# Kernel optimization log

Hardware: AMD Instinct MI355X
Metric: run time of the kernel (lower is better)

The kernel has to match this reference:

```python
import jax, jax.numpy as jnp
import numpy as np

SEQ_LEN = 64  # config.SEQ_LEN
T, B, N, D = 256, 128, 4, 2
H_HIS, H_INT = 32, 8


def _uniform(key, shape, k):
    return jax.random.uniform(key, shape, jnp.float32, -k, k)


def setup_inputs() -> dict:
    key = jax.random.key(0)
    ks = jax.random.split(key, 12)
    kh = 1.0 / np.sqrt(H_HIS)
    ki = 1.0 / np.sqrt(H_INT)
    ko = 1.0 / np.sqrt(40)
    return {
        "inputs": jax.random.normal(ks[0], (T, B, N, D), jnp.float32),
        # history LSTM (input 2 -> hidden 32), gate order i,f,g,o like torch
        "Wih_his": _uniform(ks[1], (4 * H_HIS, D), kh),
        "Whh_his": _uniform(ks[2], (4 * H_HIS, H_HIS), kh),
        "bih_his": _uniform(ks[3], (4 * H_HIS,), kh),
        "bhh_his": _uniform(ks[4], (4 * H_HIS,), kh),
        # interaction LSTM (input 2 -> hidden 8)
        "Wih_int": _uniform(ks[5], (4 * H_INT, D), ki),
        "Whh_int": _uniform(ks[6], (4 * H_INT, H_INT), ki),
        "bih_int": _uniform(ks[7], (4 * H_INT,), ki),
        "bhh_int": _uniform(ks[8], (4 * H_INT,), ki),
        # output Linear(40 -> 2)
        "W_out": _uniform(ks[9], (2, H_HIS + H_INT), ko),
        "b_out": _uniform(ks[10], (2,), ko),
    }


def _lstm_windows(x_w, valid, Wih, Whh, bih, bhh):
    """Run an LSTM over L steps for T independent windows at once.
    x_w: [L, Tw, B, d]  inputs per step (leading padding for short windows)
    valid: [L, Tw] bool; while False the state is held at zero, which is
    exactly equivalent to starting the window fresh at its first valid step.
    Returns final hidden state h: [Tw, B, H].
    """
    H = Whh.shape[1]
    Tw, Bb = x_w.shape[1], x_w.shape[2]
    b = bih + bhh

    def step(carry, xs):
        h, c = carry
        x, v = xs
        g = x @ Wih.T + h @ Whh.T + b            # [Tw, B, 4H]
        i, f, gg, o = jnp.split(g, 4, axis=-1)
        c_new = jax.nn.sigmoid(f) * c + jax.nn.sigmoid(i) * jnp.tanh(gg)
        h_new = jax.nn.sigmoid(o) * jnp.tanh(c_new)
        m = v[:, None, None]
        return (jnp.where(m, h_new, 0.0), jnp.where(m, c_new, 0.0)), None

    init = (jnp.zeros((Tw, Bb, H), x_w.dtype), jnp.zeros((Tw, Bb, H), x_w.dtype))
    (h, _), _ = jax.lax.scan(step, init, (x_w, valid))
    return h


def reference(inputs, Wih_his, Whh_his, bih_his, bhh_his,
              Wih_int, Whh_int, bih_int, bhh_int, W_out, b_out):
    Tt, Bb, Nn, Dd = inputs.shape
    L = SEQ_LEN
    # window index for output frame t: frames t-L+1 .. t (clipped; invalid masked)
    t = jnp.arange(Tt)[:, None]
    s = jnp.arange(L)[None, :]
    idx = t - (L - 1) + s                      # [T, L]
    valid = (idx >= 0)
    idx_c = jnp.clip(idx, 0, Tt - 1)
    x_his = inputs[:, :, -1, :][idx_c]         # [T, L, B, d] (ego / last node)
    x_int = inputs[:, :, 0, :][idx_c]          # [T, L, B, d] (interaction node)
    x_his = jnp.transpose(x_his, (1, 0, 2, 3))  # [L, T, B, d]
    x_int = jnp.transpose(x_int, (1, 0, 2, 3))
    v = jnp.transpose(valid)                   # [L, T]

    h_his = _lstm_windows(x_his, v, Wih_his, Whh_his, bih_his, bhh_his)  # [T,B,32]
    h_int = _lstm_windows(x_int, v, Wih_int, Whh_int, bih_int, bhh_int)  # [T,B,8]
    emb = jnp.concatenate([h_his, h_int], axis=-1)                       # [T,B,40]
    return emb @ W_out.T + b_out                                         # [T,B,2]
```

## Files before the change

kernel.cpp:

```cpp
#include <hip/hip_runtime.h>


typedef float v2f __attribute__((ext_vector_type(2)));
typedef float v4f __attribute__((ext_vector_type(4)));
typedef _Float16 h8v __attribute__((ext_vector_type(8)));

static __device__ __forceinline__ float fexp2(float x) {
    return __builtin_amdgcn_exp2f(x);
}
static __device__ __forceinline__ float frcp(float x) {
    return __builtin_amdgcn_rcpf(x);
}
static __device__ __forceinline__ unsigned short f2h(float f) {
    _Float16 h = (_Float16)f;
    unsigned short u;
    __builtin_memcpy(&u, &h, 2);
    return u;
}
static __device__ __forceinline__ float h2f(unsigned short u) {
    _Float16 h;
    __builtin_memcpy(&h, &u, 2);
    return (float)h;
}

#define LOG2E    1.442695041f
#define TWOLOG2E 2.885390082f

__global__ __launch_bounds__(256) void prep_kernel(
    const float* __restrict__ Wih_his, const float* __restrict__ Whh_his,
    const float* __restrict__ bih_his, const float* __restrict__ bhh_his,
    const float* __restrict__ Wih_int, const float* __restrict__ Whh_int,
    const float* __restrict__ bih_int, const float* __restrict__ bhh_int,
    float* __restrict__ ws)
{
    const int i = blockIdx.x * 256 + threadIdx.x;
    if (i < 4832) {
    } else if (i < 4960) {
        const int p = i - 4832;
        const int T = p >> 4, n = p & 15;
        const int gi = T >> 1, u = 2 * n + (T & 1);
        const int r = gi * 32 + u;
        const float s = (gi == 2) ? -TWOLOG2E : -LOG2E;
        ws[5120 + p] = (bih_his[r] + bhh_his[r]) * s;
    } else if (i < 5216) {
        const int e = i - 4960;
        const int p = e >> 1, comp = e & 1;
        const int T = p >> 4, n = p & 15;
        const int gi = T >> 1, u = 2 * n + (T & 1);
        const int r = gi * 32 + u;
        const float s = (gi == 2) ? -TWOLOG2E : -LOG2E;
        ws[5376 + e] = Wih_his[r * 2 + comp] * s;
    } else if (i < 9312) {
        const int e = i - 5216;
        const int p = e >> 5, k = e & 31;
        const int T = p >> 4, n = p & 15;
        const int gi = T >> 1, u = 2 * n + (T & 1);
        const int r = gi * 32 + u;
        const float s = (gi == 2) ? -TWOLOG2E : -LOG2E;
        reinterpret_cast<unsigned short*>(ws)[11776 + e] =
            f2h(Whh_his[r * 32 + k] * s);
    } else if (i < 9344) {
        const int s = i - 9312;
        const int T = s >> 4, m = s & 15, r = m & 3;
        const int gate = (4 * T + r) >> 1, unit = 2 * (m >> 2) + (r & 1);
        const int orig = gate * 8 + unit;
        const float sc = (gate == 2) ? -TWOLOG2E : -LOG2E;
        ws[7936 + s] = (bih_int[orig] + bhh_int[orig]) * sc;
    } else if (i < 9408) {
        const int e = i - 9344;
        const int s = e >> 1, comp = e & 1;
        const int T = s >> 4, m = s & 15, r = m & 3;
        const int gate = (4 * T + r) >> 1, unit = 2 * (m >> 2) + (r & 1);
        const int orig = gate * 8 + unit;
        const float sc = (gate == 2) ? -TWOLOG2E : -LOG2E;
        ws[7968 + e] = Wih_int[orig * 2 + comp] * sc;
    } else if (i < 9664) {
        const int e = i - 9408;
        const int s = e >> 3, k = e & 7;
        const int T = s >> 4, m = s & 15, r = m & 3;
        const int gate = (4 * T + r) >> 1, unit = 2 * (m >> 2) + (r & 1);
        const int orig = gate * 8 + unit;
        const float sc = (gate == 2) ? -TWOLOG2E : -LOG2E;
        const float w = Whh_int[orig * 8 + k] * sc;
        const unsigned short hi = f2h(w);
        const unsigned short lo = f2h(w - h2f(hi));
        reinterpret_cast<unsigned short*>(ws)[16128 + e] = hi;
        reinterpret_cast<unsigned short*>(ws)[8704 + e]  = lo;
    }
}

__global__ __launch_bounds__(64) void intm_kernel(
    const float* __restrict__ inp, const float* __restrict__ ws,
    const float* __restrict__ W_out, float* __restrict__ eInt)
{
    const int lane = threadIdx.x;
    const int n    = lane & 15;
    const int q    = lane >> 4;
    const int Wd   = blockIdx.x;
    const int t    = Wd >> 3;
    const int bg   = Wd & 7;
    const int nsteps = (t >= 63) ? 64 : (t + 1);
    const int tau0   = (t >= 63) ? (t - 63) : 0;

    h8v Ai[2];
    {
        const h8v* wah = reinterpret_cast<const h8v*>(
            reinterpret_cast<const unsigned short*>(ws) + 16128);
        const h8v* wal = reinterpret_cast<const h8v*>(
            reinterpret_cast<const unsigned short*>(ws) + 8704);
#pragma unroll
        for (int T = 0; T < 2; ++T) {
            const h8v vh = wah[T * 16 + n];
            const h8v vl = wal[T * 16 + n];
            Ai[T] = (q < 2) ? vh : vl;
        }
    }

    float cb[2][4], cw0v[2][4], cw1v[2][4];
#pragma unroll
    for (int T = 0; T < 2; ++T)
#pragma unroll
        for (int r = 0; r < 4; ++r) {
            const int s = T * 16 + q * 4 + r;
            cb[T][r]   = ws[7936 + s];
            cw0v[T][r] = ws[7968 + 2 * s];
            cw1v[T][r] = ws[7968 + 2 * s + 1];
        }

    const int chain = bg * 16 + n;
    const float* xp = inp + tau0 * 1024 + chain * 8;
    float2 xv = *reinterpret_cast<const float2*>(xp);
    float2 x1 = make_float2(0.f, 0.f);
    if (nsteps > 1) x1 = *reinterpret_cast<const float2*>(xp + 1024);
    xp += 2048;

    union BU { unsigned u[4]; h8v h; } bf;
    bf.u[0] = bf.u[1] = bf.u[2] = bf.u[3] = 0;

    float cI0 = 0.f, cI1 = 0.f, h0 = 0.f, h1 = 0.f;

#pragma unroll 1
    for (int s = 0; s < nsteps; ++s) {
        float2 x2 = make_float2(0.f, 0.f);
        if (s + 2 < nsteps)
            x2 = *reinterpret_cast<const float2*>(xp);
        xp += 1024;

        v4f C0, C1;
#pragma unroll
        for (int r = 0; r < 4; ++r) {
            C0[r] = fmaf(cw1v[0][r], xv.y, fmaf(cw0v[0][r], xv.x, cb[0][r]));
            C1[r] = fmaf(cw1v[1][r], xv.y, fmaf(cw0v[1][r], xv.x, cb[1][r]));
        }
        const v4f D0 = __builtin_amdgcn_mfma_f32_16x16x32_f16(Ai[0], bf.h, C0, 0, 0, 0);
        const v4f D1 = __builtin_amdgcn_mfma_f32_16x16x32_f16(Ai[1], bf.h, C1, 0, 0, 0);

        {
            const float si = frcp(1.f + fexp2(D0[0]));
            const float sf = frcp(1.f + fexp2(D0[2]));
            const float tg = fmaf(2.f, frcp(1.f + fexp2(D1[0])), -1.f);
            const float so = frcp(1.f + fexp2(D1[2]));
            const float cn = fmaf(sf, cI0, si * tg);
            cI0 = cn;
            h0 = so * fmaf(-2.f, frcp(1.f + fexp2(TWOLOG2E * cn)), 1.f);
        }
        {
            const float si = frcp(1.f + fexp2(D0[1]));
            const float sf = frcp(1.f + fexp2(D0[3]));
            const float tg = fmaf(2.f, frcp(1.f + fexp2(D1[1])), -1.f);
            const float so = frcp(1.f + fexp2(D1[3]));
            const float cn = fmaf(sf, cI1, si * tg);
            cI1 = cn;
            h1 = so * fmaf(-2.f, frcp(1.f + fexp2(TWOLOG2E * cn)), 1.f);
        }

        if (s + 1 < nsteps) {
            const unsigned short h0h = f2h(h0), h1h = f2h(h1);
            const float h0l = h0 - h2f(h0h);
            const float h1l = h1 - h2f(h1h);
            const unsigned pkh = ((unsigned)h1h << 16) | h0h;
            const unsigned pkl = ((unsigned)f2h(h1l) << 16) | f2h(h0l);
#pragma unroll
            for (int d = 0; d < 4; ++d) {
                const unsigned uh = (unsigned)__shfl((int)pkh, d * 16 + n);
                const unsigned ul = (unsigned)__shfl((int)pkl, d * 16 + n);
                bf.u[d] = (q & 1) ? ul : uh;
            }
        }

        xv = x1;
        x1 = x2;
    }

    const float wo0a = W_out[32 + 2 * q], wo0b = W_out[33 + 2 * q];
    const float wo1a = W_out[72 + 2 * q], wo1b = W_out[73 + 2 * q];
    float e0 = fmaf(wo0b, h1, wo0a * h0);
    float e1 = fmaf(wo1b, h1, wo1a * h0);
    e0 += __shfl_xor(e0, 16); e1 += __shfl_xor(e1, 16);
    e0 += __shfl_xor(e0, 32); e1 += __shfl_xor(e1, 32);
    if (lane < 16) {
        float2 o; o.x = e0; o.y = e1;
        reinterpret_cast<float2*>(eInt)[t * 128 + chain] = o;
    }
}

__global__ __launch_bounds__(64) void his_kernel(
    const float* __restrict__ inp, const float* __restrict__ ws,
    const float* __restrict__ W_out, const float* __restrict__ b_out,
    const float* __restrict__ eInt, float* __restrict__ out)
{
    __shared__ __align__(16) unsigned short hm[2][16][40];

    const int lane = threadIdx.x;
    const int n    = lane & 15;
    const int quad = lane >> 4;
    const int Wd   = blockIdx.x;
    const int t    = Wd >> 3;
    const int bg   = Wd & 7;
    const int nsteps = (t >= 63) ? 64 : (t + 1);
    const int tau0   = (t >= 63) ? (t - 63) : 0;

    h8v Bf[8];
    {
        const h8v* wb = reinterpret_cast<const h8v*>(
            reinterpret_cast<const unsigned short*>(ws) + 11776);
#pragma unroll
        for (int T = 0; T < 8; ++T) Bf[T] = wb[(T * 16 + n) * 4 + quad];
    }
    float cb[8], cw0[8], cw1[8];
#pragma unroll
    for (int T = 0; T < 8; ++T) {
        const int p = T * 16 + n;
        cb[T]  = ws[5120 + p];
        cw0[T] = ws[5376 + 2 * p];
        cw1[T] = ws[5376 + 2 * p + 1];
    }

    const int bbase = bg * 16 + quad * 4;
    const float* xp = inp + tau0 * 1024 + bbase * 8 + 6;
    float2 xc[4];
#pragma unroll
    for (int r = 0; r < 4; ++r)
        xc[r] = *reinterpret_cast<const float2*>(xp + r * 8);
    xp += 1024;

    h8v Af = {};
    float cs[4][2] = {};
    float h0[4] = {}, h1[4] = {};

#pragma unroll 1
    for (int s = 0; s < nsteps; ++s) {
        float2 xn[4];
        if (s + 1 < nsteps) {
#pragma unroll
            for (int r = 0; r < 4; ++r)
                xn[r] = *reinterpret_cast<const float2*>(xp + r * 8);
        } else {
#pragma unroll
            for (int r = 0; r < 4; ++r) xn[r] = make_float2(0.f, 0.f);
        }
        xp += 1024;

        v4f D[8];
#pragma unroll
        for (int T = 0; T < 8; ++T) {
            v4f C;
#pragma unroll
            for (int r = 0; r < 4; ++r)
                C[r] = fmaf(cw1[T], xc[r].y, fmaf(cw0[T], xc[r].x, cb[T]));
            D[T] = __builtin_amdgcn_mfma_f32_16x16x32_f16(Af, Bf[T], C, 0, 0, 0);
        }

#pragma unroll
        for (int r = 0; r < 4; ++r) {
            {
                const float si = frcp(1.f + fexp2(D[0][r]));
                const float sf = frcp(1.f + fexp2(D[2][r]));
                const float tg = fmaf(2.f, frcp(1.f + fexp2(D[4][r])), -1.f);
                const float so = frcp(1.f + fexp2(D[6][r]));
                const float cn = fmaf(sf, cs[r][0], si * tg);
                cs[r][0] = cn;
                h0[r] = so * fmaf(-2.f, frcp(1.f + fexp2(TWOLOG2E * cn)), 1.f);
            }
            {
                const float si = frcp(1.f + fexp2(D[1][r]));
                const float sf = frcp(1.f + fexp2(D[3][r]));
                const float tg = fmaf(2.f, frcp(1.f + fexp2(D[5][r])), -1.f);
                const float so = frcp(1.f + fexp2(D[7][r]));
                const float cn = fmaf(sf, cs[r][1], si * tg);
                cs[r][1] = cn;
                h1[r] = so * fmaf(-2.f, frcp(1.f + fexp2(TWOLOG2E * cn)), 1.f);
            }
        }

        if (s + 1 < nsteps) {
            const int bf = s & 1;
#pragma unroll
            for (int r = 0; r < 4; ++r) {
                const unsigned pk =
                    ((unsigned)f2h(h1[r]) << 16) | f2h(h0[r]);
                *reinterpret_cast<unsigned*>(&hm[bf][quad * 4 + r][2 * n]) = pk;
            }
            __builtin_amdgcn_wave_barrier();
            asm volatile("s_waitcnt lgkmcnt(0)" ::: "memory");
            __builtin_amdgcn_wave_barrier();
            Af = *reinterpret_cast<const h8v*>(&hm[bf][n][quad * 8]);
        }

#pragma unroll
        for (int r = 0; r < 4; ++r) xc[r] = xn[r];
    }

    const float wo0a = W_out[2 * n],      wo0b = W_out[2 * n + 1];
    const float wo1a = W_out[40 + 2 * n], wo1b = W_out[40 + 2 * n + 1];
    float e0[4], e1[4];
#pragma unroll
    for (int r = 0; r < 4; ++r) {
        e0[r] = fmaf(wo0b, h1[r], wo0a * h0[r]);
        e1[r] = fmaf(wo1b, h1[r], wo1a * h0[r]);
#pragma unroll
        for (int m = 1; m <= 8; m <<= 1) {
            e0[r] += __shfl_xor(e0[r], m);
            e1[r] += __shfl_xor(e1[r], m);
        }
    }
    if (n == 0) {
        const float bo0 = b_out[0], bo1 = b_out[1];
#pragma unroll
        for (int r = 0; r < 4; ++r) {
            const int chain = t * 128 + bbase + r;
            const float2 ei = reinterpret_cast<const float2*>(eInt)[chain];
            float2 o;
            o.x = e0[r] + ei.x + bo0;
            o.y = e1[r] + ei.y + bo1;
            reinterpret_cast<float2*>(out)[chain] = o;
        }
    }
}

extern "C" void kernel_launch(void* const* d_in, const int* in_sizes, int n_in,
                              void* d_out, int out_size, void* d_ws, size_t ws_size,
                              hipStream_t stream) {
    const float* inp     = (const float*)d_in[0];
    const float* Wih_his = (const float*)d_in[1];
    const float* Whh_his = (const float*)d_in[2];
    const float* bih_his = (const float*)d_in[3];
    const float* bhh_his = (const float*)d_in[4];
    const float* Wih_int = (const float*)d_in[5];
    const float* Whh_int = (const float*)d_in[6];
    const float* bih_int = (const float*)d_in[7];
    const float* bhh_int = (const float*)d_in[8];
    const float* W_out   = (const float*)d_in[9];
    const float* b_out   = (const float*)d_in[10];
    float* out  = (float*)d_out;
    float* ws   = (float*)d_ws;
    float* eInt = ws + 8192;

    prep_kernel<<<dim3(38), dim3(256), 0, stream>>>(
        Wih_his, Whh_his, bih_his, bhh_his,
        Wih_int, Whh_int, bih_int, bhh_int, ws);

    intm_kernel<<<dim3(2048), dim3(64), 0, stream>>>(inp, ws, W_out, eInt);

    his_kernel<<<dim3(2048), dim3(64), 0, stream>>>(
        inp, ws, W_out, b_out, eInt, out);
}
```

Baseline: 197.9 us.

## Fuse interaction LSTM into history LSTM kernel to share launch and overlap chains

Merges the separate interaction-LSTM kernel into the history-LSTM kernel so each wave runs both recurrences in the same step loop. The interaction embedding is combined through lane shuffles instead of a global scratch round trip. This removes one kernel launch and lets the independent interaction MFMA/transcendental chain fill latency gaps in the history chain. It raises register pressure per wave, which may reduce occupancy or lengthen each step.

```diff
diff --git a/kernel.cpp b/kernel.cpp
--- a/kernel.cpp
+++ b/kernel.cpp
@@ -89,125 +89,10 @@
     }
 }
 
-__global__ __launch_bounds__(64) void intm_kernel(
-    const float* __restrict__ inp, const float* __restrict__ ws,
-    const float* __restrict__ W_out, float* __restrict__ eInt)
-{
-    const int lane = threadIdx.x;
-    const int n    = lane & 15;
-    const int q    = lane >> 4;
-    const int Wd   = blockIdx.x;
-    const int t    = Wd >> 3;
-    const int bg   = Wd & 7;
-    const int nsteps = (t >= 63) ? 64 : (t + 1);
-    const int tau0   = (t >= 63) ? (t - 63) : 0;
-
-    h8v Ai[2];
-    {
-        const h8v* wah = reinterpret_cast<const h8v*>(
-            reinterpret_cast<const unsigned short*>(ws) + 16128);
-        const h8v* wal = reinterpret_cast<const h8v*>(
-            reinterpret_cast<const unsigned short*>(ws) + 8704);
-#pragma unroll
-        for (int T = 0; T < 2; ++T) {
-            const h8v vh = wah[T * 16 + n];
-            const h8v vl = wal[T * 16 + n];
-            Ai[T] = (q < 2) ? vh : vl;
-        }
-    }
-
-    float cb[2][4], cw0v[2][4], cw1v[2][4];
-#pragma unroll
-    for (int T = 0; T < 2; ++T)
-#pragma unroll
-        for (int r = 0; r < 4; ++r) {
-            const int s = T * 16 + q * 4 + r;
-            cb[T][r]   = ws[7936 + s];
-            cw0v[T][r] = ws[7968 + 2 * s];
-            cw1v[T][r] = ws[7968 + 2 * s + 1];
-        }
-
-    const int chain = bg * 16 + n;
-    const float* xp = inp + tau0 * 1024 + chain * 8;
-    float2 xv = *reinterpret_cast<const float2*>(xp);
-    float2 x1 = make_float2(0.f, 0.f);
-    if (nsteps > 1) x1 = *reinterpret_cast<const float2*>(xp + 1024);
-    xp += 2048;
-
-    union BU { unsigned u[4]; h8v h; } bf;
-    bf.u[0] = bf.u[1] = bf.u[2] = bf.u[3] = 0;
-
-    float cI0 = 0.f, cI1 = 0.f, h0 = 0.f, h1 = 0.f;
-
-#pragma unroll 1
-    for (int s = 0; s < nsteps; ++s) {
-        float2 x2 = make_float2(0.f, 0.f);
-        if (s + 2 < nsteps)
-            x2 = *reinterpret_cast<const float2*>(xp);
-        xp += 1024;
-
-        v4f C0, C1;
-#pragma unroll
-        for (int r = 0; r < 4; ++r) {
-            C0[r] = fmaf(cw1v[0][r], xv.y, fmaf(cw0v[0][r], xv.x, cb[0][r]));
-            C1[r] = fmaf(cw1v[1][r], xv.y, fmaf(cw0v[1][r], xv.x, cb[1][r]));
-        }
-        const v4f D0 = __builtin_amdgcn_mfma_f32_16x16x32_f16(Ai[0], bf.h, C0, 0, 0, 0);
-        const v4f D1 = __builtin_amdgcn_mfma_f32_16x16x32_f16(Ai[1], bf.h, C1, 0, 0, 0);
-
-        {
-            const float si = frcp(1.f + fexp2(D0[0]));
-            const float sf = frcp(1.f + fexp2(D0[2]));
-            const float tg = fmaf(2.f, frcp(1.f + fexp2(D1[0])), -1.f);
-            const float so = frcp(1.f + fexp2(D1[2]));
-            const float cn = fmaf(sf, cI0, si * tg);
-            cI0 = cn;
-            h0 = so * fmaf(-2.f, frcp(1.f + fexp2(TWOLOG2E * cn)), 1.f);
-        }
-        {
-            const float si = frcp(1.f + fexp2(D0[1]));
-            const float sf = frcp(1.f + fexp2(D0[3]));
-            const float tg = fmaf(2.f, frcp(1.f + fexp2(D1[1])), -1.f);
-            const float so = frcp(1.f + fexp2(D1[3]));
-            const float cn = fmaf(sf, cI1, si * tg);
-            cI1 = cn;
-            h1 = so * fmaf(-2.f, frcp(1.f + fexp2(TWOLOG2E * cn)), 1.f);
-        }
-
-        if (s + 1 < nsteps) {
-            const unsigned short h0h = f2h(h0), h1h = f2h(h1);
-            const float h0l = h0 - h2f(h0h);
-            const float h1l = h1 - h2f(h1h);
-            const unsigned pkh = ((unsigned)h1h << 16) | h0h;
-            const unsigned pkl = ((unsigned)f2h(h1l) << 16) | f2h(h0l);
-#pragma unroll
-            for (int d = 0; d < 4; ++d) {
-                const unsigned uh = (unsigned)__shfl((int)pkh, d * 16 + n);
-                const unsigned ul = (unsigned)__shfl((int)pkl, d * 16 + n);
-                bf.u[d] = (q & 1) ? ul : uh;
-            }
-        }
-
-        xv = x1;
-        x1 = x2;
-    }
-
-    const float wo0a = W_out[32 + 2 * q], wo0b = W_out[33 + 2 * q];
-    const float wo1a = W_out[72 + 2 * q], wo1b = W_out[73 + 2 * q];
-    float e0 = fmaf(wo0b, h1, wo0a * h0);
-    float e1 = fmaf(wo1b, h1, wo1a * h0);
-    e0 += __shfl_xor(e0, 16); e1 += __shfl_xor(e1, 16);
-    e0 += __shfl_xor(e0, 32); e1 += __shfl_xor(e1, 32);
-    if (lane < 16) {
-        float2 o; o.x = e0; o.y = e1;
-        reinterpret_cast<float2*>(eInt)[t * 128 + chain] = o;
-    }
-}
-
-__global__ __launch_bounds__(64) void his_kernel(
+__global__ __launch_bounds__(64) void fused_kernel(
     const float* __restrict__ inp, const float* __restrict__ ws,
     const float* __restrict__ W_out, const float* __restrict__ b_out,
-    const float* __restrict__ eInt, float* __restrict__ out)
+    float* __restrict__ out)
 {
     __shared__ __align__(16) unsigned short hm[2][16][40];
 
@@ -236,6 +121,30 @@
         cw1[T] = ws[5376 + 2 * p + 1];
     }
 
+    h8v Ai[2];
+    {
+        const h8v* wah = reinterpret_cast<const h8v*>(
+            reinterpret_cast<const unsigned short*>(ws) + 16128);
+        const h8v* wal = reinterpret_cast<const h8v*>(
+            reinterpret_cast<const unsigned short*>(ws) + 8704);
+#pragma unroll
+        for (int T = 0; T < 2; ++T) {
+            const h8v vh = wah[T * 16 + n];
+            const h8v vl = wal[T * 16 + n];
+            Ai[T] = (quad < 2) ? vh : vl;
+        }
+    }
+    float icb[2][4], icw0[2][4], icw1[2][4];
+#pragma unroll
+    for (int T = 0; T < 2; ++T)
+#pragma unroll
+        for (int r = 0; r < 4; ++r) {
+            const int s = T * 16 + quad * 4 + r;
+            icb[T][r]  = ws[7936 + s];
+            icw0[T][r] = ws[7968 + 2 * s];
+            icw1[T][r] = ws[7968 + 2 * s + 1];
+        }
+
     const int bbase = bg * 16 + quad * 4;
     const float* xp = inp + tau0 * 1024 + bbase * 8 + 6;
     float2 xc[4];
@@ -244,22 +153,33 @@
         xc[r] = *reinterpret_cast<const float2*>(xp + r * 8);
     xp += 1024;
 
+    const int ichain = bg * 16 + n;
+    const float* ixp = inp + tau0 * 1024 + ichain * 8;
+    float2 ixv = *reinterpret_cast<const float2*>(ixp);
+    ixp += 1024;
+
     h8v Af = {};
     float cs[4][2] = {};
     float h0[4] = {}, h1[4] = {};
+    union BU { unsigned u[4]; h8v h; } bfr;
+    bfr.u[0] = bfr.u[1] = bfr.u[2] = bfr.u[3] = 0;
+    float cI0 = 0.f, cI1 = 0.f, ih0 = 0.f, ih1 = 0.f;
 
 #pragma unroll 1
     for (int s = 0; s < nsteps; ++s) {
         float2 xn[4];
+        float2 ixn = make_float2(0.f, 0.f);
         if (s + 1 < nsteps) {
 #pragma unroll
             for (int r = 0; r < 4; ++r)
                 xn[r] = *reinterpret_cast<const float2*>(xp + r * 8);
+            ixn = *reinterpret_cast<const float2*>(ixp);
         } else {
 #pragma unroll
             for (int r = 0; r < 4; ++r) xn[r] = make_float2(0.f, 0.f);
         }
         xp += 1024;
+        ixp += 1024;
 
         v4f D[8];
 #pragma unroll
@@ -269,6 +189,37 @@
             for (int r = 0; r < 4; ++r)
                 C[r] = fmaf(cw1[T], xc[r].y, fmaf(cw0[T], xc[r].x, cb[T]));
             D[T] = __builtin_amdgcn_mfma_f32_16x16x32_f16(Af, Bf[T], C, 0, 0, 0);
+        }
+
+        v4f iD0, iD1;
+        {
+            v4f C0, C1;
+#pragma unroll
+            for (int r = 0; r < 4; ++r) {
+                C0[r] = fmaf(icw1[0][r], ixv.y, fmaf(icw0[0][r], ixv.x, icb[0][r]));
+                C1[r] = fmaf(icw1[1][r], ixv.y, fmaf(icw0[1][r], ixv.x, icb[1][r]));
+            }
+            iD0 = __builtin_amdgcn_mfma_f32_16x16x32_f16(Ai[0], bfr.h, C0, 0, 0, 0);
+            iD1 = __builtin_amdgcn_mfma_f32_16x16x32_f16(Ai[1], bfr.h, C1, 0, 0, 0);
+        }
+
+        {
+            const float si = frcp(1.f + fexp2(iD0[0]));
+            const float sf = frcp(1.f + fexp2(iD0[2]));
+            const float tg = fmaf(2.f, frcp(1.f + fexp2(iD1[0])), -1.f);
+            const float so = frcp(1.f + fexp2(iD1[2]));
+            const float cn = fmaf(sf, cI0, si * tg);
+            cI0 = cn;
+            ih0 = so * fmaf(-2.f, frcp(1.f + fexp2(TWOLOG2E * cn)), 1.f);
+        }
+        {
+            const float si = frcp(1.f + fexp2(iD0[1]));
+            const float sf = frcp(1.f + fexp2(iD0[3]));
+            const float tg = fmaf(2.f, frcp(1.f + fexp2(iD1[1])), -1.f);
+            const float so = frcp(1.f + fexp2(iD1[3]));
+            const float cn = fmaf(sf, cI1, si * tg);
+            cI1 = cn;
+            ih1 = so * fmaf(-2.f, frcp(1.f + fexp2(TWOLOG2E * cn)), 1.f);
         }
 
 #pragma unroll
@@ -294,21 +245,45 @@
         }
 
         if (s + 1 < nsteps) {
-            const int bf = s & 1;
+            {
+                const unsigned short h0h = f2h(ih0), h1h = f2h(ih1);
+                const float h0l = ih0 - h2f(h0h);
+                const float h1l = ih1 - h2f(h1h);
+                const unsigned pkh = ((unsigned)h1h << 16) | h0h;
+                const unsigned pkl = ((unsigned)f2h(h1l) << 16) | f2h(h0l);
+#pragma unroll
+                for (int d = 0; d < 4; ++d) {
+                    const unsigned uh = (unsigned)__shfl((int)pkh, d * 16 + n);
+                    const unsigned ul = (unsigned)__shfl((int)pkl, d * 16 + n);
+                    bfr.u[d] = (quad & 1) ? ul : uh;
+                }
+            }
+            const int bfi = s & 1;
 #pragma unroll
             for (int r = 0; r < 4; ++r) {
                 const unsigned pk =
                     ((unsigned)f2h(h1[r]) << 16) | f2h(h0[r]);
-                *reinterpret_cast<unsigned*>(&hm[bf][quad * 4 + r][2 * n]) = pk;
+                *reinterpret_cast<unsigned*>(&hm[bfi][quad * 4 + r][2 * n]) = pk;
             }
             __builtin_amdgcn_wave_barrier();
             asm volatile("s_waitcnt lgkmcnt(0)" ::: "memory");
             __builtin_amdgcn_wave_barrier();
-            Af = *reinterpret_cast<const h8v*>(&hm[bf][n][quad * 8]);
+            Af = *reinterpret_cast<const h8v*>(&hm[bfi][n][quad * 8]);
         }
 
 #pragma unroll
         for (int r = 0; r < 4; ++r) xc[r] = xn[r];
+        ixv = ixn;
+    }
+
+    float ie0, ie1;
+    {
+        const float wo0a = W_out[32 + 2 * quad], wo0b = W_out[33 + 2 * quad];
+        const float wo1a = W_out[72 + 2 * quad], wo1b = W_out[73 + 2 * quad];
+        ie0 = fmaf(wo0b, ih1, wo0a * ih0);
+        ie1 = fmaf(wo1b, ih1, wo1a * ih0);
+        ie0 += __shfl_xor(ie0, 16); ie1 += __shfl_xor(ie1, 16);
+        ie0 += __shfl_xor(ie0, 32); ie1 += __shfl_xor(ie1, 32);
     }
 
     const float wo0a = W_out[2 * n],      wo0b = W_out[2 * n + 1];
@@ -324,15 +299,22 @@
             e1[r] += __shfl_xor(e1[r], m);
         }
     }
+
+    float g0[4], g1[4];
+#pragma unroll
+    for (int r = 0; r < 4; ++r) {
+        g0[r] = __shfl(ie0, quad * 4 + r);
+        g1[r] = __shfl(ie1, quad * 4 + r);
+    }
+
     if (n == 0) {
         const float bo0 = b_out[0], bo1 = b_out[1];
 #pragma unroll
         for (int r = 0; r < 4; ++r) {
             const int chain = t * 128 + bbase + r;
-            const float2 ei = reinterpret_cast<const float2*>(eInt)[chain];
             float2 o;
-            o.x = e0[r] + ei.x + bo0;
-            o.y = e1[r] + ei.y + bo1;
+            o.x = e0[r] + g0[r] + bo0;
+            o.y = e1[r] + g1[r] + bo1;
             reinterpret_cast<float2*>(out)[chain] = o;
         }
     }
@@ -354,14 +336,11 @@
     const float* b_out   = (const float*)d_in[10];
     float* out  = (float*)d_out;
     float* ws   = (float*)d_ws;
-    float* eInt = ws + 8192;
 
     prep_kernel<<<dim3(38), dim3(256), 0, stream>>>(
         Wih_his, Whh_his, bih_his, bhh_his,
         Wih_int, Whh_int, bih_int, bhh_int, ws);
 
-    intm_kernel<<<dim3(2048), dim3(64), 0, stream>>>(inp, ws, W_out, eInt);
-
-    his_kernel<<<dim3(2048), dim3(64), 0, stream>>>(
-        inp, ws, W_out, b_out, eInt, out);
-}
+    fused_kernel<<<dim3(2048), dim3(64), 0, stream>>>(
+        inp, ws, W_out, b_out, out);
+}
```

Result: slower. 238.3 us (+20.4%).

## Swap MFMA operand roles and fold input/bias projection into MFMAs

Applied to the files above, without the earlier changes.

Both LSTM kernels now put weights in the A operand and the hidden state in the B operand, so each lane keeps its own chain's hidden units in registers. The history kernel no longer needs the LDS round trip and wave barriers between steps, and the interaction kernel no longer needs the per-step lane shuffles. The input and bias terms are also computed by extra MFMAs against hi/lo fp16-split inputs with a constant-one column, replacing the per-step scalar FMAs. The cost is twice as many MFMAs per step in the history kernel and more fp16 splitting work per step, with some precision risk from fp16 hi/lo splitting.

```diff
diff --git a/kernel.cpp b/kernel.cpp
--- a/kernel.cpp
+++ b/kernel.cpp
@@ -1,7 +1,6 @@
 #include <hip/hip_runtime.h>
 
 
-typedef float v2f __attribute__((ext_vector_type(2)));
 typedef float v4f __attribute__((ext_vector_type(4)));
 typedef _Float16 h8v __attribute__((ext_vector_type(8)));
 
@@ -25,6 +24,7 @@
 
 #define LOG2E    1.442695041f
 #define TWOLOG2E 2.885390082f
+#define H16ONE   0x3C00u
 
 __global__ __launch_bounds__(256) void prep_kernel(
     const float* __restrict__ Wih_his, const float* __restrict__ Whh_his,
@@ -34,62 +34,68 @@
     float* __restrict__ ws)
 {
     const int i = blockIdx.x * 256 + threadIdx.x;
-    if (i < 4832) {
-    } else if (i < 4960) {
-        const int p = i - 4832;
-        const int T = p >> 4, n = p & 15;
-        const int gi = T >> 1, u = 2 * n + (T & 1);
-        const int r = gi * 32 + u;
-        const float s = (gi == 2) ? -TWOLOG2E : -LOG2E;
-        ws[5120 + p] = (bih_his[r] + bhh_his[r]) * s;
-    } else if (i < 5216) {
-        const int e = i - 4960;
-        const int p = e >> 1, comp = e & 1;
-        const int T = p >> 4, n = p & 15;
-        const int gi = T >> 1, u = 2 * n + (T & 1);
-        const int r = gi * 32 + u;
-        const float s = (gi == 2) ? -TWOLOG2E : -LOG2E;
-        ws[5376 + e] = Wih_his[r * 2 + comp] * s;
-    } else if (i < 9312) {
-        const int e = i - 5216;
-        const int p = e >> 5, k = e & 31;
-        const int T = p >> 4, n = p & 15;
-        const int gi = T >> 1, u = 2 * n + (T & 1);
-        const int r = gi * 32 + u;
-        const float s = (gi == 2) ? -TWOLOG2E : -LOG2E;
-        reinterpret_cast<unsigned short*>(ws)[11776 + e] =
-            f2h(Whh_his[r * 32 + k] * s);
-    } else if (i < 9344) {
-        const int s = i - 9312;
-        const int T = s >> 4, m = s & 15, r = m & 3;
-        const int gate = (4 * T + r) >> 1, unit = 2 * (m >> 2) + (r & 1);
-        const int orig = gate * 8 + unit;
-        const float sc = (gate == 2) ? -TWOLOG2E : -LOG2E;
-        ws[7936 + s] = (bih_int[orig] + bhh_int[orig]) * sc;
-    } else if (i < 9408) {
-        const int e = i - 9344;
-        const int s = e >> 1, comp = e & 1;
-        const int T = s >> 4, m = s & 15, r = m & 3;
-        const int gate = (4 * T + r) >> 1, unit = 2 * (m >> 2) + (r & 1);
-        const int orig = gate * 8 + unit;
-        const float sc = (gate == 2) ? -TWOLOG2E : -LOG2E;
-        ws[7968 + e] = Wih_int[orig * 2 + comp] * sc;
-    } else if (i < 9664) {
-        const int e = i - 9408;
-        const int s = e >> 3, k = e & 7;
-        const int T = s >> 4, m = s & 15, r = m & 3;
-        const int gate = (4 * T + r) >> 1, unit = 2 * (m >> 2) + (r & 1);
-        const int orig = gate * 8 + unit;
-        const float sc = (gate == 2) ? -TWOLOG2E : -LOG2E;
-        const float w = Whh_int[orig * 8 + k] * sc;
-        const unsigned short hi = f2h(w);
-        const unsigned short lo = f2h(w - h2f(hi));
-        reinterpret_cast<unsigned short*>(ws)[16128 + e] = hi;
-        reinterpret_cast<unsigned short*>(ws)[8704 + e]  = lo;
-    }
-}
-
-__global__ __launch_bounds__(64) void intm_kernel(
+    unsigned short* wsu = reinterpret_cast<unsigned short*>(ws);
+
+    if (i < 4096) {
+        const int T = i >> 9, m = (i >> 5) & 15, k = i & 31;
+        const int g = T >> 1;
+        const int u = ((m >> 2) << 3) + ((T & 1) << 2) + (m & 3);
+        const int orig = g * 32 + u;
+        const float s = (g == 2) ? -TWOLOG2E : -LOG2E;
+        wsu[i] = f2h(Whh_his[orig * 32 + k] * s);
+    } else if (i < 8192) {
+        const int e = i - 4096;
+        const int T = e >> 9, m = (e >> 5) & 15, k = e & 31;
+        const int g = T >> 1;
+        const int u = ((m >> 2) << 3) + ((T & 1) << 2) + (m & 3);
+        const int orig = g * 32 + u;
+        const float s = (g == 2) ? -TWOLOG2E : -LOG2E;
+        const float w0 = Wih_his[orig * 2] * s;
+        const float w1 = Wih_his[orig * 2 + 1] * s;
+        const float b  = (bih_his[orig] + bhh_his[orig]) * s;
+        unsigned short v = 0;
+        switch (k) {
+            case 0: v = f2h(w0); break;
+            case 1: v = f2h(w1); break;
+            case 2: v = f2h(b);  break;
+            case 3: v = f2h(w0 - h2f(f2h(w0))); break;
+            case 4: v = f2h(w1 - h2f(f2h(w1))); break;
+            case 5: v = f2h(b  - h2f(f2h(b)));  break;
+            case 6: v = f2h(w0); break;
+            case 7: v = f2h(w1); break;
+            default: v = 0; break;
+        }
+        wsu[4096 + e] = v;
+    } else if (i < 9216) {
+        const int e = i - 8192;
+        const int T = e >> 9, m = (e >> 5) & 15, k = e & 31;
+        const int q = k >> 3, j = k & 7;
+        const int g = 2 * T + ((m & 3) >> 1);
+        const int u = 2 * (m >> 2) + (m & 1);
+        const int orig = g * 8 + u;
+        const float s = (g == 2) ? -TWOLOG2E : -LOG2E;
+        unsigned short v = 0;
+        if (j < 6) {
+            const int col = 2 * q + (j & 1);
+            const float w = Whh_int[orig * 8 + col] * s;
+            v = (j == 2 || j == 3) ? f2h(w - h2f(f2h(w))) : f2h(w);
+        } else {
+            const int comp = j & 1;
+            if (q <= 1) {
+                v = f2h(Wih_int[orig * 2 + comp] * s);
+            } else if (q == 2) {
+                const float w = Wih_int[orig * 2 + comp] * s;
+                v = f2h(w - h2f(f2h(w)));
+            } else {
+                const float b = (bih_int[orig] + bhh_int[orig]) * s;
+                v = (comp == 0) ? f2h(b) : f2h(b - h2f(f2h(b)));
+            }
+        }
+        wsu[8192 + e] = v;
+    }
+}
+
+__global__ __launch_bounds__(64) void intw_kernel(
     const float* __restrict__ inp, const float* __restrict__ ws,
     const float* __restrict__ W_out, float* __restrict__ eInt)
 {
@@ -102,58 +108,42 @@
     const int nsteps = (t >= 63) ? 64 : (t + 1);
     const int tau0   = (t >= 63) ? (t - 63) : 0;
 
-    h8v Ai[2];
-    {
-        const h8v* wah = reinterpret_cast<const h8v*>(
-            reinterpret_cast<const unsigned short*>(ws) + 16128);
-        const h8v* wal = reinterpret_cast<const h8v*>(
-            reinterpret_cast<const unsigned short*>(ws) + 8704);
-#pragma unroll
-        for (int T = 0; T < 2; ++T) {
-            const h8v vh = wah[T * 16 + n];
-            const h8v vl = wal[T * 16 + n];
-            Ai[T] = (q < 2) ? vh : vl;
-        }
-    }
-
-    float cb[2][4], cw0v[2][4], cw1v[2][4];
-#pragma unroll
-    for (int T = 0; T < 2; ++T)
-#pragma unroll
-        for (int r = 0; r < 4; ++r) {
-            const int s = T * 16 + q * 4 + r;
-            cb[T][r]   = ws[7936 + s];
-            cw0v[T][r] = ws[7968 + 2 * s];
-            cw1v[T][r] = ws[7968 + 2 * s + 1];
-        }
+    const unsigned short* wsu = reinterpret_cast<const unsigned short*>(ws);
+    const h8v* wa = reinterpret_cast<const h8v*>(wsu + 8192);
+    h8v AI[2];
+#pragma unroll
+    for (int T = 0; T < 2; ++T) AI[T] = wa[T * 64 + n * 4 + q];
 
     const int chain = bg * 16 + n;
     const float* xp = inp + tau0 * 1024 + chain * 8;
     float2 xv = *reinterpret_cast<const float2*>(xp);
-    float2 x1 = make_float2(0.f, 0.f);
-    if (nsteps > 1) x1 = *reinterpret_cast<const float2*>(xp + 1024);
-    xp += 2048;
-
-    union BU { unsigned u[4]; h8v h; } bf;
-    bf.u[0] = bf.u[1] = bf.u[2] = bf.u[3] = 0;
-
-    float cI0 = 0.f, cI1 = 0.f, h0 = 0.f, h1 = 0.f;
+    xp += 1024;
+
+    union BU { unsigned u[4]; h8v h; } bh;
+    bh.u[0] = bh.u[1] = bh.u[2] = bh.u[3] = 0;
+
+    float cI0 = 0.f, cI1 = 0.f, ih0 = 0.f, ih1 = 0.f;
 
 #pragma unroll 1
     for (int s = 0; s < nsteps; ++s) {
-        float2 x2 = make_float2(0.f, 0.f);
-        if (s + 2 < nsteps)
-            x2 = *reinterpret_cast<const float2*>(xp);
+        float2 xn = make_float2(0.f, 0.f);
+        if (s + 1 < nsteps)
+            xn = *reinterpret_cast<const float2*>(xp);
         xp += 1024;
 
-        v4f C0, C1;
-#pragma unroll
-        for (int r = 0; r < 4; ++r) {
-            C0[r] = fmaf(cw1v[0][r], xv.y, fmaf(cw0v[0][r], xv.x, cb[0][r]));
-            C1[r] = fmaf(cw1v[1][r], xv.y, fmaf(cw0v[1][r], xv.x, cb[1][r]));
-        }
-        const v4f D0 = __builtin_amdgcn_mfma_f32_16x16x32_f16(Ai[0], bf.h, C0, 0, 0, 0);
-        const v4f D1 = __builtin_amdgcn_mfma_f32_16x16x32_f16(Ai[1], bf.h, C1, 0, 0, 0);
+        {
+            const unsigned short xh = f2h(xv.x), yh = f2h(xv.y);
+            const unsigned short xl = f2h(xv.x - h2f(xh));
+            const unsigned short yl = f2h(xv.y - h2f(yh));
+            const unsigned pkh = ((unsigned)yh << 16) | xh;
+            const unsigned pkl = ((unsigned)yl << 16) | xl;
+            bh.u[3] = (q == 3) ? ((H16ONE << 16) | H16ONE)
+                               : ((q == 1) ? pkl : pkh);
+        }
+
+        const v4f z = {0.f, 0.f, 0.f, 0.f};
+        const v4f D0 = __builtin_amdgcn_mfma_f32_16x16x32_f16(AI[0], bh.h, z, 0, 0, 0);
+        const v4f D1 = __builtin_amdgcn_mfma_f32_16x16x32_f16(AI[1], bh.h, z, 0, 0, 0);
 
         {
             const float si = frcp(1.f + fexp2(D0[0]));
@@ -162,7 +152,7 @@
             const float so = frcp(1.f + fexp2(D1[2]));
             const float cn = fmaf(sf, cI0, si * tg);
             cI0 = cn;
-            h0 = so * fmaf(-2.f, frcp(1.f + fexp2(TWOLOG2E * cn)), 1.f);
+            ih0 = so * fmaf(-2.f, frcp(1.f + fexp2(TWOLOG2E * cn)), 1.f);
         }
         {
             const float si = frcp(1.f + fexp2(D0[1]));
@@ -171,31 +161,25 @@
             const float so = frcp(1.f + fexp2(D1[3]));
             const float cn = fmaf(sf, cI1, si * tg);
             cI1 = cn;
-            h1 = so * fmaf(-2.f, frcp(1.f + fexp2(TWOLOG2E * cn)), 1.f);
-        }
-
-        if (s + 1 < nsteps) {
-            const unsigned short h0h = f2h(h0), h1h = f2h(h1);
-            const float h0l = h0 - h2f(h0h);
-            const float h1l = h1 - h2f(h1h);
-            const unsigned pkh = ((unsigned)h1h << 16) | h0h;
-            const unsigned pkl = ((unsigned)f2h(h1l) << 16) | f2h(h0l);
-#pragma unroll
-            for (int d = 0; d < 4; ++d) {
-                const unsigned uh = (unsigned)__shfl((int)pkh, d * 16 + n);
-                const unsigned ul = (unsigned)__shfl((int)pkl, d * 16 + n);
-                bf.u[d] = (q & 1) ? ul : uh;
-            }
-        }
-
-        xv = x1;
-        x1 = x2;
+            ih1 = so * fmaf(-2.f, frcp(1.f + fexp2(TWOLOG2E * cn)), 1.f);
+        }
+
+        {
+            const unsigned short hh0 = f2h(ih0), hh1 = f2h(ih1);
+            const unsigned short hl0 = f2h(ih0 - h2f(hh0));
+            const unsigned short hl1 = f2h(ih1 - h2f(hh1));
+            bh.u[0] = ((unsigned)hh1 << 16) | hh0;
+            bh.u[1] = bh.u[0];
+            bh.u[2] = ((unsigned)hl1 << 16) | hl0;
+        }
+
+        xv = xn;
     }
 
     const float wo0a = W_out[32 + 2 * q], wo0b = W_out[33 + 2 * q];
     const float wo1a = W_out[72 + 2 * q], wo1b = W_out[73 + 2 * q];
-    float e0 = fmaf(wo0b, h1, wo0a * h0);
-    float e1 = fmaf(wo1b, h1, wo1a * h0);
+    float e0 = fmaf(wo0b, ih1, wo0a * ih0);
+    float e1 = fmaf(wo1b, ih1, wo1a * ih0);
     e0 += __shfl_xor(e0, 16); e1 += __shfl_xor(e1, 16);
     e0 += __shfl_xor(e0, 32); e1 += __shfl_xor(e1, 32);
     if (lane < 16) {
@@ -204,137 +188,108 @@
     }
 }
 
-__global__ __launch_bounds__(64) void his_kernel(
+__global__ __launch_bounds__(64) void hisw_kernel(
     const float* __restrict__ inp, const float* __restrict__ ws,
     const float* __restrict__ W_out, const float* __restrict__ b_out,
     const float* __restrict__ eInt, float* __restrict__ out)
 {
-    __shared__ __align__(16) unsigned short hm[2][16][40];
-
     const int lane = threadIdx.x;
     const int n    = lane & 15;
-    const int quad = lane >> 4;
+    const int q    = lane >> 4;
     const int Wd   = blockIdx.x;
     const int t    = Wd >> 3;
     const int bg   = Wd & 7;
     const int nsteps = (t >= 63) ? 64 : (t + 1);
     const int tau0   = (t >= 63) ? (t - 63) : 0;
 
-    h8v Bf[8];
-    {
-        const h8v* wb = reinterpret_cast<const h8v*>(
-            reinterpret_cast<const unsigned short*>(ws) + 11776);
-#pragma unroll
-        for (int T = 0; T < 8; ++T) Bf[T] = wb[(T * 16 + n) * 4 + quad];
-    }
-    float cb[8], cw0[8], cw1[8];
+    const unsigned short* wsu = reinterpret_cast<const unsigned short*>(ws);
+    const h8v* wa = reinterpret_cast<const h8v*>(wsu);
+    const h8v* wx = reinterpret_cast<const h8v*>(wsu + 4096);
+    h8v AW[8], AX[8];
 #pragma unroll
     for (int T = 0; T < 8; ++T) {
-        const int p = T * 16 + n;
-        cb[T]  = ws[5120 + p];
-        cw0[T] = ws[5376 + 2 * p];
-        cw1[T] = ws[5376 + 2 * p + 1];
-    }
-
-    const int bbase = bg * 16 + quad * 4;
-    const float* xp = inp + tau0 * 1024 + bbase * 8 + 6;
-    float2 xc[4];
-#pragma unroll
-    for (int r = 0; r < 4; ++r)
-        xc[r] = *reinterpret_cast<const float2*>(xp + r * 8);
+        AW[T] = wa[T * 64 + n * 4 + q];
+        AX[T] = wx[T * 64 + n * 4 + q];
+    }
+
+    const int chain = bg * 16 + n;
+    const float* xp = inp + tau0 * 1024 + chain * 8 + 6;
+    float2 xv = *reinterpret_cast<const float2*>(xp);
     xp += 1024;
 
-    h8v Af = {};
-    float cs[4][2] = {};
-    float h0[4] = {}, h1[4] = {};
+    union BU { unsigned u[4]; h8v h; } bh;
+    bh.u[0] = bh.u[1] = bh.u[2] = bh.u[3] = 0;
+    float c[8] = {0.f, 0.f, 0.f, 0.f, 0.f, 0.f, 0.f, 0.f};
+    float h[8] = {0.f, 0.f, 0.f, 0.f, 0.f, 0.f, 0.f, 0.f};
 
 #pragma unroll 1
     for (int s = 0; s < nsteps; ++s) {
-        float2 xn[4];
-        if (s + 1 < nsteps) {
-#pragma unroll
-            for (int r = 0; r < 4; ++r)
-                xn[r] = *reinterpret_cast<const float2*>(xp + r * 8);
-        } else {
-#pragma unroll
-            for (int r = 0; r < 4; ++r) xn[r] = make_float2(0.f, 0.f);
-        }
+        float2 xn = make_float2(0.f, 0.f);
+        if (s + 1 < nsteps)
+            xn = *reinterpret_cast<const float2*>(xp);
         xp += 1024;
 
+        union BU bx;
+        {
+            const unsigned short xh = f2h(xv.x), yh = f2h(xv.y);
+            const unsigned short xl = f2h(xv.x - h2f(xh));
+            const unsigned short yl = f2h(xv.y - h2f(yh));
+            bx.u[0] = ((unsigned)yh << 16) | xh;
+            bx.u[1] = ((unsigned)xh << 16) | H16ONE;
+            bx.u[2] = (H16ONE << 16) | yh;
+            bx.u[3] = ((unsigned)yl << 16) | xl;
+            if (q != 0) { bx.u[0] = 0; bx.u[1] = 0; bx.u[2] = 0; bx.u[3] = 0; }
+        }
+
+        const v4f z = {0.f, 0.f, 0.f, 0.f};
         v4f D[8];
 #pragma unroll
         for (int T = 0; T < 8; ++T) {
-            v4f C;
-#pragma unroll
-            for (int r = 0; r < 4; ++r)
-                C[r] = fmaf(cw1[T], xc[r].y, fmaf(cw0[T], xc[r].x, cb[T]));
-            D[T] = __builtin_amdgcn_mfma_f32_16x16x32_f16(Af, Bf[T], C, 0, 0, 0);
-        }
-
-#pragma unroll
-        for (int r = 0; r < 4; ++r) {
-            {
-                const float si = frcp(1.f + fexp2(D[0][r]));
-                const float sf = frcp(1.f + fexp2(D[2][r]));
-                const float tg = fmaf(2.f, frcp(1.f + fexp2(D[4][r])), -1.f);
-                const float so = frcp(1.f + fexp2(D[6][r]));
-                const float cn = fmaf(sf, cs[r][0], si * tg);
-                cs[r][0] = cn;
-                h0[r] = so * fmaf(-2.f, frcp(1.f + fexp2(TWOLOG2E * cn)), 1.f);
+            const v4f cx = __builtin_amdgcn_mfma_f32_16x16x32_f16(AX[T], bx.h, z, 0, 0, 0);
+            D[T] = __builtin_amdgcn_mfma_f32_16x16x32_f16(AW[T], bh.h, cx, 0, 0, 0);
+        }
+
+#pragma unroll
+        for (int hi = 0; hi < 2; ++hi) {
+#pragma unroll
+            for (int lo = 0; lo < 4; ++lo) {
+                const int ww = hi * 4 + lo;
+                const float si = frcp(1.f + fexp2(D[hi][lo]));
+                const float sf = frcp(1.f + fexp2(D[2 + hi][lo]));
+                const float tg = fmaf(2.f, frcp(1.f + fexp2(D[4 + hi][lo])), -1.f);
+                const float so = frcp(1.f + fexp2(D[6 + hi][lo]));
+                const float cn = fmaf(sf, c[ww], si * tg);
+                c[ww] = cn;
+                h[ww] = so * fmaf(-2.f, frcp(1.f + fexp2(TWOLOG2E * cn)), 1.f);
             }
-            {
-                const float si = frcp(1.f + fexp2(D[1][r]));
-                const float sf = frcp(1.f + fexp2(D[3][r]));
-                const float tg = fmaf(2.f, frcp(1.f + fexp2(D[5][r])), -1.f);
-                const float so = frcp(1.f + fexp2(D[7][r]));
-                const float cn = fmaf(sf, cs[r][1], si * tg);
-                cs[r][1] = cn;
-                h1[r] = so * fmaf(-2.f, frcp(1.f + fexp2(TWOLOG2E * cn)), 1.f);
-            }
-        }
-
-        if (s + 1 < nsteps) {
-            const int bf = s & 1;
-#pragma unroll
-            for (int r = 0; r < 4; ++r) {
-                const unsigned pk =
-                    ((unsigned)f2h(h1[r]) << 16) | f2h(h0[r]);
-                *reinterpret_cast<unsigned*>(&hm[bf][quad * 4 + r][2 * n]) = pk;
-            }
-            __builtin_amdgcn_wave_barrier();
-            asm volatile("s_waitcnt lgkmcnt(0)" ::: "memory");
-            __builtin_amdgcn_wave_barrier();
-            Af = *reinterpret_cast<const h8v*>(&hm[bf][n][quad * 8]);
-        }
-
-#pragma unroll
-        for (int r = 0; r < 4; ++r) xc[r] = xn[r];
-    }
-
-    const float wo0a = W_out[2 * n],      wo0b = W_out[2 * n + 1];
-    const float wo1a = W_out[40 + 2 * n], wo1b = W_out[40 + 2 * n + 1];
-    float e0[4], e1[4];
-#pragma unroll
-    for (int r = 0; r < 4; ++r) {
-        e0[r] = fmaf(wo0b, h1[r], wo0a * h0[r]);
-        e1[r] = fmaf(wo1b, h1[r], wo1a * h0[r]);
-#pragma unroll
-        for (int m = 1; m <= 8; m <<= 1) {
-            e0[r] += __shfl_xor(e0[r], m);
-            e1[r] += __shfl_xor(e1[r], m);
-        }
-    }
-    if (n == 0) {
-        const float bo0 = b_out[0], bo1 = b_out[1];
-#pragma unroll
-        for (int r = 0; r < 4; ++r) {
-            const int chain = t * 128 + bbase + r;
-            const float2 ei = reinterpret_cast<const float2*>(eInt)[chain];
-            float2 o;
-            o.x = e0[r] + ei.x + bo0;
-            o.y = e1[r] + ei.y + bo1;
-            reinterpret_cast<float2*>(out)[chain] = o;
-        }
+        }
+
+#pragma unroll
+        for (int d = 0; d < 4; ++d)
+            bh.u[d] = ((unsigned)f2h(h[2 * d + 1]) << 16) | f2h(h[2 * d]);
+
+        xv = xn;
+    }
+
+    const v4f w0a = *reinterpret_cast<const v4f*>(W_out + q * 8);
+    const v4f w0b = *reinterpret_cast<const v4f*>(W_out + q * 8 + 4);
+    const v4f w1a = *reinterpret_cast<const v4f*>(W_out + 40 + q * 8);
+    const v4f w1b = *reinterpret_cast<const v4f*>(W_out + 40 + q * 8 + 4);
+    float e0 = 0.f, e1 = 0.f;
+#pragma unroll
+    for (int j = 0; j < 4; ++j) {
+        e0 = fmaf(w0a[j], h[j], fmaf(w0b[j], h[4 + j], e0));
+        e1 = fmaf(w1a[j], h[j], fmaf(w1b[j], h[4 + j], e1));
+    }
+    e0 += __shfl_xor(e0, 16); e1 += __shfl_xor(e1, 16);
+    e0 += __shfl_xor(e0, 32); e1 += __shfl_xor(e1, 32);
+
+    if (lane < 16) {
+        const float2 ei = reinterpret_cast<const float2*>(eInt)[t * 128 + chain];
+        float2 o;
+        o.x = e0 + ei.x + b_out[0];
+        o.y = e1 + ei.y + b_out[1];
+        reinterpret_cast<float2*>(out)[t * 128 + chain] = o;
     }
 }
 
@@ -356,12 +311,12 @@
     float* ws   = (float*)d_ws;
     float* eInt = ws + 8192;
 
-    prep_kernel<<<dim3(38), dim3(256), 0, stream>>>(
+    prep_kernel<<<dim3(36), dim3(256), 0, stream>>>(
         Wih_his, Whh_his, bih_his, bhh_his,
         Wih_int, Whh_int, bih_int, bhh_int, ws);
 
-    intm_kernel<<<dim3(2048), dim3(64), 0, stream>>>(inp, ws, W_out, eInt);
-
-    his_kernel<<<dim3(2048), dim3(64), 0, stream>>>(
+    intw_kernel<<<dim3(2048), dim3(64), 0, stream>>>(inp, ws, W_out, eInt);
+
+    hisw_kernel<<<dim3(2048), dim3(64), 0, stream>>>(
         inp, ws, W_out, b_out, eInt, out);
 }
```

New measurement: 185.9 us. 6.1% less time.
